# Kernel optimization log

Hardware: AMD Instinct MI355X
Metric: run time of the kernel (lower is better)

The kernel has to match this reference:

```python
import jax, jax.numpy as jnp
import numpy as np

N_CELLS = 50000
DEG = 32
NNZ = N_CELLS * DEG
D_IN = 64
D_OUT = 64
NEG_SLOPE = 0.2


def setup_inputs() -> dict:
    key = jax.random.key(0)
    k0, k1, k2, k3, k4 = jax.random.split(key, 5)
    x_source = jax.random.normal(k0, (N_CELLS, D_IN), jnp.float32)
    # COO indices of the sparse neighborhood matrix N: DEG entries per row
    edge_rows = jnp.repeat(jnp.arange(N_CELLS, dtype=jnp.int32), DEG)
    edge_cols = jax.random.randint(k1, (NNZ,), 0, N_CELLS, dtype=jnp.int32)
    neighborhood_values = jax.random.uniform(k2, (NNZ,), jnp.float32)
    # xavier_uniform-ish scales (exact init irrelevant for correctness baseline)
    W0 = jax.random.normal(k3, (D_IN, D_OUT), jnp.float32) * (1.414 / np.sqrt(D_IN))
    a0 = jax.random.normal(k4, (2 * D_OUT, 1), jnp.float32) * 0.1
    return {
        "x_source": x_source,
        "edge_rows": edge_rows,
        "edge_cols": edge_cols,
        "neighborhood_values": neighborhood_values,
        "W0": W0,
        "a0": a0,
    }


def reference(x_source, edge_rows, edge_cols, neighborhood_values, W0, a0):
    # message = X W_p  : [n_cells, d_out]
    message = x_source @ W0
    d = message.shape[1]
    # [X_i || X_j] a  ==  (X_i a_src) + (X_j a_dst); compute node-level dot first,
    # then gather per edge (avoids materializing [nnz, 2d] concat)
    a_src = a0[:d, 0]
    a_dst = a0[d:, 0]
    node_src = message @ a_src  # [n_cells]
    node_dst = message @ a_dst  # [n_cells]
    e = jax.nn.leaky_relu(node_src[edge_rows] + node_dst[edge_cols],
                          negative_slope=NEG_SLOPE)  # [nnz]
    # sparse_row_norm: divide each edge value by its row sum (softmax=False path)
    row_sum = jax.ops.segment_sum(e, edge_rows, num_segments=N_CELLS)
    att = e / row_sum[edge_rows]
    # Hadamard product N^1 \odot A_1, then SpMM with message
    vals = neighborhood_values * att  # [nnz]
    out = jax.ops.segment_sum(vals[:, None] * message[edge_cols], edge_rows,
                              num_segments=N_CELLS)  # [n_cells, d_out]
    # update_func='relu'
    return jax.nn.relu(out)
```

## Files before the change

kernel.cpp:

```cpp
#include <hip/hip_runtime.h>
#include <hip/hip_fp16.h>

#define N_CELLS 50000
#define DEG 32
#define DIM 64
#define NEG_SLOPE 0.2
#define NPAIRS (N_CELLS / 2)

__global__ __launch_bounds__(256)
void gat_prep(const float* __restrict__ x,
              const float* __restrict__ W0,
              const float* __restrict__ a0,
              __half* __restrict__ x2,
              double* __restrict__ ns,
              double* __restrict__ nd) {
  __shared__ double2 p_s[DIM];

  const int tid = threadIdx.x;
  if (tid < DIM) {
    double ps = 0.0, pd = 0.0;
    const float4* w4 = (const float4*)(W0 + tid * DIM);
#pragma unroll
    for (int q = 0; q < DIM / 4; ++q) {
      float4 w = w4[q];
      ps = fma((double)w.x, (double)a0[4 * q + 0], ps);
      ps = fma((double)w.y, (double)a0[4 * q + 1], ps);
      ps = fma((double)w.z, (double)a0[4 * q + 2], ps);
      ps = fma((double)w.w, (double)a0[4 * q + 3], ps);
      pd = fma((double)w.x, (double)a0[DIM + 4 * q + 0], pd);
      pd = fma((double)w.y, (double)a0[DIM + 4 * q + 1], pd);
      pd = fma((double)w.z, (double)a0[DIM + 4 * q + 2], pd);
      pd = fma((double)w.w, (double)a0[DIM + 4 * q + 3], pd);
    }
    p_s[tid] = make_double2(ps, pd);
  }
  __syncthreads();

  const int r = blockIdx.x * 256 + tid;
  if (r >= N_CELLS) return;

  const float4* x4 = (const float4*)(x + (size_t)r * DIM);
  double s0 = 0.0, s1 = 0.0, d0 = 0.0, d1 = 0.0;
  __half2 hbuf[DIM / 2];
#pragma unroll
  for (int q = 0; q < DIM / 4; ++q) {
    float4 v = x4[q];
    double2 p0 = p_s[4 * q + 0], p1 = p_s[4 * q + 1];
    double2 p2 = p_s[4 * q + 2], p3 = p_s[4 * q + 3];
    s0 = fma((double)v.x, p0.x, s0); d0 = fma((double)v.x, p0.y, d0);
    s1 = fma((double)v.y, p1.x, s1); d1 = fma((double)v.y, p1.y, d1);
    s0 = fma((double)v.z, p2.x, s0); d0 = fma((double)v.z, p2.y, d0);
    s1 = fma((double)v.w, p3.x, s1); d1 = fma((double)v.w, p3.y, d1);
    hbuf[2 * q + 0] = __float22half2_rn(make_float2(v.x, v.y));
    hbuf[2 * q + 1] = __float22half2_rn(make_float2(v.z, v.w));
  }
  ns[r] = s0 + s1;
  nd[r] = d0 + d1;

  const uint4* src = (const uint4*)hbuf;
  uint4* p2v = (uint4*)(x2 + (size_t)r * DIM);
#pragma unroll
  for (int i = 0; i < 8; ++i) p2v[i] = src[i];
}

__global__ __launch_bounds__(256, 4)
void gat_edges(const __half* __restrict__ x2,
               const int* __restrict__ ecol,
               const float* __restrict__ nv,
               const float* __restrict__ W0,
               const double* __restrict__ ns,
               const double* __restrict__ nd,
               float* __restrict__ out) {
  __shared__ __align__(16) float w_s[4][2][DEG];
  __shared__ __align__(16) int c_s[4][2][DEG];
  __shared__ __align__(16) float h_s[4][2][2][DIM];

  const int lane = threadIdx.x & 63;
  const int wid = threadIdx.x >> 6;
  const int half = lane >> 5;
  const int sub = lane & 31;

  float w0c[DIM];
#pragma unroll
  for (int k = 0; k < DIM; ++k) w0c[k] = W0[k * DIM + lane];

  const int gwave = blockIdx.x * 4 + wid;
  const int nwaves = gridDim.x * 4;
  const unsigned* xp = (const unsigned*)x2;

  int buf = 0;
  for (int p = gwave; p < NPAIRS; p += nwaves, buf ^= 1) {
    const int r0 = 2 * p;

    const int eidx = r0 * DEG + lane;
    const int col = __builtin_nontemporal_load(ecol + eidx);
    const float nvv = __builtin_nontemporal_load(nv + eidx);
    double z = ns[r0 + half] + nd[col];
    double e = (z >= 0.0) ? z : NEG_SLOPE * z;
    double rs = e;
#pragma unroll
    for (int m = 16; m >= 1; m >>= 1) rs += __shfl_xor(rs, m, 64);
    w_s[wid][half][sub] = (float)((double)nvv * (e / rs));
    c_s[wid][half][sub] = col;

    const int* cs = c_s[wid][half];
    const float* wsp = w_s[wid][half];
    float ax = 0.0f, ay = 0.0f;
#pragma unroll
    for (int q0 = 0; q0 < DEG; q0 += 8) {
      const int4 ca = ((const int4*)(cs + q0))[0];
      const int4 cb = ((const int4*)(cs + q0))[1];
      const float4 wa = ((const float4*)(wsp + q0))[0];
      const float4 wb = ((const float4*)(wsp + q0))[1];
      unsigned pk0 = xp[(size_t)ca.x * (DIM / 2) + sub];
      unsigned pk1 = xp[(size_t)ca.y * (DIM / 2) + sub];
      unsigned pk2 = xp[(size_t)ca.z * (DIM / 2) + sub];
      unsigned pk3 = xp[(size_t)ca.w * (DIM / 2) + sub];
      unsigned pk4 = xp[(size_t)cb.x * (DIM / 2) + sub];
      unsigned pk5 = xp[(size_t)cb.y * (DIM / 2) + sub];
      unsigned pk6 = xp[(size_t)cb.z * (DIM / 2) + sub];
      unsigned pk7 = xp[(size_t)cb.w * (DIM / 2) + sub];
      float2 v0 = __half22float2(*(const __half2*)&pk0);
      float2 v1 = __half22float2(*(const __half2*)&pk1);
      float2 v2 = __half22float2(*(const __half2*)&pk2);
      float2 v3 = __half22float2(*(const __half2*)&pk3);
      float2 v4 = __half22float2(*(const __half2*)&pk4);
      float2 v5 = __half22float2(*(const __half2*)&pk5);
      float2 v6 = __half22float2(*(const __half2*)&pk6);
      float2 v7 = __half22float2(*(const __half2*)&pk7);
      ax = fmaf(wa.x, v0.x, ax); ay = fmaf(wa.x, v0.y, ay);
      ax = fmaf(wa.y, v1.x, ax); ay = fmaf(wa.y, v1.y, ay);
      ax = fmaf(wa.z, v2.x, ax); ay = fmaf(wa.z, v2.y, ay);
      ax = fmaf(wa.w, v3.x, ax); ay = fmaf(wa.w, v3.y, ay);
      ax = fmaf(wb.x, v4.x, ax); ay = fmaf(wb.x, v4.y, ay);
      ax = fmaf(wb.y, v5.x, ax); ay = fmaf(wb.y, v5.y, ay);
      ax = fmaf(wb.z, v6.x, ax); ay = fmaf(wb.z, v6.y, ay);
      ax = fmaf(wb.w, v7.x, ax); ay = fmaf(wb.w, v7.y, ay);
    }
    ((float2*)h_s[wid][buf][half])[sub] = make_float2(ax, ay);

    float oA = 0.0f, oB = 0.0f;
    const float4* hA = (const float4*)h_s[wid][buf][0];
    const float4* hB = (const float4*)h_s[wid][buf][1];
#pragma unroll
    for (int q = 0; q < DIM / 4; ++q) {
      float4 a = hA[q];
      float4 b = hB[q];
      oA = fmaf(a.x, w0c[4 * q + 0], oA); oB = fmaf(b.x, w0c[4 * q + 0], oB);
      oA = fmaf(a.y, w0c[4 * q + 1], oA); oB = fmaf(b.y, w0c[4 * q + 1], oB);
      oA = fmaf(a.z, w0c[4 * q + 2], oA); oB = fmaf(b.z, w0c[4 * q + 2], oB);
      oA = fmaf(a.w, w0c[4 * q + 3], oA); oB = fmaf(b.w, w0c[4 * q + 3], oB);
    }
    __builtin_nontemporal_store(fmaxf(oA, 0.0f), out + (size_t)r0 * DIM + lane);
    __builtin_nontemporal_store(fmaxf(oB, 0.0f), out + (size_t)(r0 + 1) * DIM + lane);
  }
}

extern "C" void kernel_launch(void* const* d_in, const int* in_sizes, int n_in,
                              void* d_out, int out_size, void* d_ws, size_t ws_size,
                              hipStream_t stream) {
  const float* x = (const float*)d_in[0];
  const int* ecol = (const int*)d_in[2];
  const float* nv = (const float*)d_in[3];
  const float* W0 = (const float*)d_in[4];
  const float* a0 = (const float*)d_in[5];
  float* out = (float*)d_out;

  __half* x2 = (__half*)d_ws;
  double* ns = (double*)((char*)d_ws + (size_t)N_CELLS * DIM * sizeof(__half));
  double* nd = ns + N_CELLS;

  hipLaunchKernelGGL(gat_prep, dim3((N_CELLS + 255) / 256), dim3(256), 0, stream,
                     x, W0, a0, x2, ns, nd);
  hipLaunchKernelGGL(gat_edges, dim3(1280), dim3(256), 0, stream,
                     x2, ecol, nv, W0, ns, nd, out);
}
```

Measured before the change: 123.3 us.

## Prefetch next pair's edge data and batch gathers in groups of sixteen

Software-pipelines the per-pair edge metadata: the column indices, neighborhood values and source scores for the next pair are loaded while the current pair is being processed, and the dependent nd gather is issued after the feature aggregation. The gather loop now issues sixteen independent row loads before consuming any, which raises memory-level parallelism. The attention normalization divide moves from double to float. These changes increase register pressure and slightly change numerics.

```diff
diff --git a/kernel.cpp b/kernel.cpp
--- a/kernel.cpp
+++ b/kernel.cpp
@@ -88,56 +88,58 @@
   const int nwaves = gridDim.x * 4;
   const unsigned* xp = (const unsigned*)x2;
 
+  int col_c = 0; float nv_c = 0.0f; double nd_c = 0.0, ns_c = 0.0;
+  if (gwave < NPAIRS) {
+    const int eidx = 2 * gwave * DEG + lane;
+    col_c = __builtin_nontemporal_load(ecol + eidx);
+    nv_c = __builtin_nontemporal_load(nv + eidx);
+    nd_c = nd[col_c];
+    ns_c = ns[2 * gwave + half];
+  }
+
   int buf = 0;
   for (int p = gwave; p < NPAIRS; p += nwaves, buf ^= 1) {
     const int r0 = 2 * p;
+    const int col = col_c;
+    const float nvv = nv_c;
+    const double ndv = nd_c;
+    const double nsv = ns_c;
 
-    const int eidx = r0 * DEG + lane;
-    const int col = __builtin_nontemporal_load(ecol + eidx);
-    const float nvv = __builtin_nontemporal_load(nv + eidx);
-    double z = ns[r0 + half] + nd[col];
+    double z = nsv + ndv;
     double e = (z >= 0.0) ? z : NEG_SLOPE * z;
     double rs = e;
 #pragma unroll
     for (int m = 16; m >= 1; m >>= 1) rs += __shfl_xor(rs, m, 64);
-    w_s[wid][half][sub] = (float)((double)nvv * (e / rs));
+    w_s[wid][half][sub] = nvv * ((float)e / (float)rs);
     c_s[wid][half][sub] = col;
+
+    const int pn = p + nwaves;
+    const int psafe = (pn < NPAIRS) ? pn : p;
+    const int eidxn = 2 * psafe * DEG + lane;
+    col_c = __builtin_nontemporal_load(ecol + eidxn);
+    nv_c = __builtin_nontemporal_load(nv + eidxn);
+    ns_c = ns[2 * psafe + half];
 
     const int* cs = c_s[wid][half];
     const float* wsp = w_s[wid][half];
     float ax = 0.0f, ay = 0.0f;
 #pragma unroll
-    for (int q0 = 0; q0 < DEG; q0 += 8) {
-      const int4 ca = ((const int4*)(cs + q0))[0];
-      const int4 cb = ((const int4*)(cs + q0))[1];
-      const float4 wa = ((const float4*)(wsp + q0))[0];
-      const float4 wb = ((const float4*)(wsp + q0))[1];
-      unsigned pk0 = xp[(size_t)ca.x * (DIM / 2) + sub];
-      unsigned pk1 = xp[(size_t)ca.y * (DIM / 2) + sub];
-      unsigned pk2 = xp[(size_t)ca.z * (DIM / 2) + sub];
-      unsigned pk3 = xp[(size_t)ca.w * (DIM / 2) + sub];
-      unsigned pk4 = xp[(size_t)cb.x * (DIM / 2) + sub];
-      unsigned pk5 = xp[(size_t)cb.y * (DIM / 2) + sub];
-      unsigned pk6 = xp[(size_t)cb.z * (DIM / 2) + sub];
-      unsigned pk7 = xp[(size_t)cb.w * (DIM / 2) + sub];
-      float2 v0 = __half22float2(*(const __half2*)&pk0);
-      float2 v1 = __half22float2(*(const __half2*)&pk1);
-      float2 v2 = __half22float2(*(const __half2*)&pk2);
-      float2 v3 = __half22float2(*(const __half2*)&pk3);
-      float2 v4 = __half22float2(*(const __half2*)&pk4);
-      float2 v5 = __half22float2(*(const __half2*)&pk5);
-      float2 v6 = __half22float2(*(const __half2*)&pk6);
-      float2 v7 = __half22float2(*(const __half2*)&pk7);
-      ax = fmaf(wa.x, v0.x, ax); ay = fmaf(wa.x, v0.y, ay);
-      ax = fmaf(wa.y, v1.x, ax); ay = fmaf(wa.y, v1.y, ay);
-      ax = fmaf(wa.z, v2.x, ax); ay = fmaf(wa.z, v2.y, ay);
-      ax = fmaf(wa.w, v3.x, ax); ay = fmaf(wa.w, v3.y, ay);
-      ax = fmaf(wb.x, v4.x, ax); ay = fmaf(wb.x, v4.y, ay);
-      ax = fmaf(wb.y, v5.x, ax); ay = fmaf(wb.y, v5.y, ay);
-      ax = fmaf(wb.z, v6.x, ax); ay = fmaf(wb.z, v6.y, ay);
-      ax = fmaf(wb.w, v7.x, ax); ay = fmaf(wb.w, v7.y, ay);
+    for (int b = 0; b < DEG; b += 16) {
+      unsigned pk[16];
+#pragma unroll
+      for (int i = 0; i < 16; ++i)
+        pk[i] = xp[(size_t)cs[b + i] * (DIM / 2) + sub];
+#pragma unroll
+      for (int i = 0; i < 16; ++i) {
+        float2 v = __half22float2(*(const __half2*)&pk[i]);
+        float w = wsp[b + i];
+        ax = fmaf(w, v.x, ax);
+        ay = fmaf(w, v.y, ay);
+      }
     }
     ((float2*)h_s[wid][buf][half])[sub] = make_float2(ax, ay);
+
+    nd_c = nd[col_c];
 
     float oA = 0.0f, oB = 0.0f;
     const float4* hA = (const float4*)h_s[wid][buf][0];
```

Result: faster. 120.6 us (-2.2%).
